# Performance work log

Measured on AMD Instinct MI355X. Metric: run time of the kernel, lower is better.

Reference implementation:

```python
import jax, jax.numpy as jnp
import numpy as np

# LSNNParameters defaults (norse-style)
ALPHA = 100.0            # surrogate sharpness
DT = 1e-3
TAU_SYN_INV = 1.0 / 0.005   # 200
TAU_MEM_INV = 1.0 / 0.01    # 100
TAU_ADAPT_INV = 1.0 / 800.0
V_LEAK = 0.0
V_RESET = 0.0
BETA = 1.8
VTH = 1.0                # sp.vth_init / v_th default


@jax.custom_vjp
def superspike(x):
    # Heaviside forward, SuperSpike surrogate backward ('super' method)
    return (x > 0).astype(x.dtype)

def _ss_fwd(x):
    return superspike(x), x

def _ss_bwd(x, g):
    return (g / (ALPHA * jnp.abs(x) + 1.0) ** 2,)

superspike.defvjp(_ss_fwd, _ss_bwd)


def lsnn_scan(x, w_in, w_rec):
    # x: [T, B, N_in]; w_in: [H, N_in]; w_rec: [H, H]
    T, B, _ = x.shape
    H = w_in.shape[0]
    z0 = jnp.zeros((B, H), x.dtype)
    v0 = jnp.full((B, H), V_LEAK, x.dtype)
    i0 = jnp.zeros((B, H), x.dtype)
    b0 = jnp.full((B, H), VTH, x.dtype)  # mean(v_th)

    def step(carry, xt):
        z, v, i, b = carry
        v_dec = v + DT * TAU_MEM_INV * (V_LEAK - v + i)
        i_dec = i - DT * TAU_SYN_INV * i
        b_dec = b + DT * TAU_ADAPT_INV * (VTH - b)
        z_new = superspike(v_dec - b_dec)
        zd = jax.lax.stop_gradient(z_new)  # reset/adaptation use detached spike
        v_new = (1.0 - zd) * v_dec + zd * V_RESET
        i_new = i_dec + xt @ w_in.T + z @ w_rec.T
        b_new = b_dec + zd * BETA
        return (z_new, v_new, i_new, b_new), z_new

    (zf, vf, i_f, bf), outs = jax.lax.scan(step, (z0, v0, i0, b0), x)
    return outs, (zf, vf, i_f, bf)


def setup_inputs() -> dict:
    key = jax.random.key(0)
    k1, k2, k3 = jax.random.split(key, 3)
    T, B, N_IN, H = 512, 64, 512, 1024
    x = jax.random.normal(k1, (T, B, N_IN), jnp.float32)
    w_in = jax.random.normal(k2, (H, N_IN), jnp.float32) * np.float32(np.sqrt(2.0 / H))
    w_rec = jax.random.normal(k3, (H, H), jnp.float32) * np.float32(np.sqrt(2.0 / H))
    w_rec = w_rec * (1.0 - jnp.eye(H, dtype=jnp.float32))  # autapses=False
    return {"input_tensor": x, "input_weights": w_in, "recurrent_weights": w_rec}


def reference(input_tensor, input_weights, recurrent_weights):
    return lsnn_scan(input_tensor, input_weights, recurrent_weights)
```

## Files before the change

### kernel.cpp

```cpp
#include <hip/hip_runtime.h>

typedef float f32x4 __attribute__((ext_vector_type(4)));

#define T_STEPS 512
#define BATCH   64
#define NIN     512
#define H       1024
#define BH      (BATCH * H)

#define BM 128
#define BN 128
#define BK 16
#define LDSS 132

__global__ void transpose1024(const float* __restrict__ in, float* __restrict__ out) {
    __shared__ float tile[32][33];
    const int tx = threadIdx.x, ty = threadIdx.y;
    const int xg = blockIdx.x * 32 + tx;
    const int ybase = blockIdx.y * 32;
#pragma unroll
    for (int r = 0; r < 32; r += 8)
        tile[ty + r][tx] = in[(size_t)(ybase + ty + r) * H + xg];
    __syncthreads();
    const int x2 = blockIdx.y * 32 + tx;
    const int y2base = blockIdx.x * 32;
#pragma unroll
    for (int r = 0; r < 32; r += 8)
        out[(size_t)(y2base + ty + r) * H + x2] = tile[tx][ty + r];
}

__global__ __launch_bounds__(256) void gemm_xwin(const float* __restrict__ x,
                                                 const float* __restrict__ w,
                                                 float* __restrict__ cur) {
    __shared__ __align__(16) float As[BK][LDSS];
    __shared__ __align__(16) float Bs[BK][LDSS];
    const int tid = threadIdx.x;
    const int tx = tid & 15, ty = tid >> 4;
    const int tx4 = tx * 4, ty4 = ty * 4;
    const int m0 = blockIdx.y * BM;
    const int n0 = blockIdx.x * BN;

    float acc[8][8];
#pragma unroll
    for (int i = 0; i < 8; ++i)
#pragma unroll
        for (int j = 0; j < 8; ++j) acc[i][j] = 0.0f;

    const int ar = tid >> 2;
    const int akc = (tid & 3) * 4;

    for (int k0 = 0; k0 < NIN; k0 += BK) {
        const float4 a0 = *reinterpret_cast<const float4*>(&x[(size_t)(m0 + ar) * NIN + k0 + akc]);
        const float4 a1 = *reinterpret_cast<const float4*>(&x[(size_t)(m0 + ar + 64) * NIN + k0 + akc]);
        const float4 b0 = *reinterpret_cast<const float4*>(&w[(size_t)(n0 + ar) * NIN + k0 + akc]);
        const float4 b1 = *reinterpret_cast<const float4*>(&w[(size_t)(n0 + ar + 64) * NIN + k0 + akc]);
        __syncthreads();
        As[akc + 0][ar] = a0.x; As[akc + 1][ar] = a0.y; As[akc + 2][ar] = a0.z; As[akc + 3][ar] = a0.w;
        As[akc + 0][ar + 64] = a1.x; As[akc + 1][ar + 64] = a1.y; As[akc + 2][ar + 64] = a1.z; As[akc + 3][ar + 64] = a1.w;
        Bs[akc + 0][ar] = b0.x; Bs[akc + 1][ar] = b0.y; Bs[akc + 2][ar] = b0.z; Bs[akc + 3][ar] = b0.w;
        Bs[akc + 0][ar + 64] = b1.x; Bs[akc + 1][ar + 64] = b1.y; Bs[akc + 2][ar + 64] = b1.z; Bs[akc + 3][ar + 64] = b1.w;
        __syncthreads();

#pragma unroll
        for (int kk = 0; kk < BK; ++kk) {
            const float4 av0 = *reinterpret_cast<const float4*>(&As[kk][ty4]);
            const float4 av1 = *reinterpret_cast<const float4*>(&As[kk][ty4 + 64]);
            const float4 bv0 = *reinterpret_cast<const float4*>(&Bs[kk][tx4]);
            const float4 bv1 = *reinterpret_cast<const float4*>(&Bs[kk][tx4 + 64]);
            const float ar_[8] = {av0.x, av0.y, av0.z, av0.w, av1.x, av1.y, av1.z, av1.w};
            const float br_[8] = {bv0.x, bv0.y, bv0.z, bv0.w, bv1.x, bv1.y, bv1.z, bv1.w};
#pragma unroll
            for (int i = 0; i < 8; ++i)
#pragma unroll
                for (int j = 0; j < 8; ++j)
                    acc[i][j] = fmaf(ar_[i], br_[j], acc[i][j]);
        }
    }

#pragma unroll
    for (int gi = 0; gi < 2; ++gi)
#pragma unroll
        for (int ii = 0; ii < 4; ++ii) {
            const int i = gi * 4 + ii;
            const int row = m0 + ty4 + ii + gi * 64;
            float* dst = &cur[(size_t)row * H + n0 + tx4];
            *reinterpret_cast<float4*>(dst)      = make_float4(acc[i][0], acc[i][1], acc[i][2], acc[i][3]);
            *reinterpret_cast<float4*>(dst + 64) = make_float4(acc[i][4], acc[i][5], acc[i][6], acc[i][7]);
        }
}

__global__ __launch_bounds__(256, 1) void lsnn_scan_kernel(float* __restrict__ io,
                                                           const float* __restrict__ wrecT) {
    const int tid = threadIdx.x;
    const int wave = tid >> 6, lane = tid & 63;
    const int j0 = tid * 4;
    const int wq = wave * 256;
    const int b = blockIdx.x;

    __shared__ __align__(16) float ring[3][4][1024];
    __shared__ __align__(16) int list[2][1088];
    __shared__ __align__(16) int cnt[2][4];

    float sv0 = 0.f, sv1 = 0.f, sv2 = 0.f, sv3 = 0.f;
    float si0 = 0.f, si1 = 0.f, si2 = 0.f, si3 = 0.f;
    float sb0 = 1.f, sb1 = 1.f, sb2 = 1.f, sb3 = 1.f;
    float sz0 = 0.f, sz1 = 0.f, sz2 = 0.f, sz3 = 0.f;
    int p = 0;
    int n_carry = 0;

    const float C_MEM = (float)(1e-3 * 100.0);
    const float C_SYN = (float)(1e-3 * 200.0);
    const float C_AD  = (float)(1e-3 * (1.0 / 800.0));
    const float BETA  = 1.8f;

    float* base = io + (size_t)b * H + j0;

    f32x4 P0 = *reinterpret_cast<const f32x4*>(base + (size_t)0 * BH);
    f32x4 P1 = *reinterpret_cast<const f32x4*>(base + (size_t)1 * BH);
    f32x4 P2 = *reinterpret_cast<const f32x4*>(base + (size_t)2 * BH);
    f32x4 P3 = *reinterpret_cast<const f32x4*>(base + (size_t)3 * BH);
    f32x4 P4 = *reinterpret_cast<const f32x4*>(base + (size_t)4 * BH);
    f32x4 P5 = *reinterpret_cast<const f32x4*>(base + (size_t)5 * BH);
    f32x4 P6 = *reinterpret_cast<const f32x4*>(base + (size_t)6 * BH);
    f32x4 P7 = *reinterpret_cast<const f32x4*>(base + (size_t)7 * BH);

#define STAGE(G, SLOT)                                                        \
  { const int A0s_ = (G) << 2;                                                \
    _Pragma("unroll")                                                         \
    for (int rr_ = 0; rr_ < 4; ++rr_) {                                       \
      const int ps_ = A0s_ + rr_;                                             \
      int hs_ = lst[ps_];                                                     \
      hs_ = (ps_ < n) ? hs_ : 0;                                              \
      const float* gp_ = wrecT + (size_t)(unsigned)hs_ * H + wq + lane * 4;   \
      __builtin_amdgcn_global_load_lds(                                       \
          (const __attribute__((address_space(1))) unsigned int*)gp_,         \
          (__attribute__((address_space(3))) unsigned int*)&ring[SLOT][rr_][wq], \
          16, 0, 0);                                                          \
    } }

#define SCAN_STEP(T, CREG, PF)                                                \
  {                                                                           \
    const float cc0 = CREG.x, cc1 = CREG.y, cc2 = CREG.z, cc3 = CREG.w;       \
    const int n = __builtin_amdgcn_readfirstlane(n_carry);                    \
    const int NT = (n + 3) >> 2;                                              \
    const int* lst = &list[p][0];                                             \
     \
    if (NT > 0) STAGE(0, 0);                                                  \
    if (NT > 1) STAGE(1, 1);                                                  \
    if (NT > 2) STAGE(2, 2);                                                  \
                                  \
    const float vd0 = sv0 + C_MEM * (0.0f - sv0 + si0);                       \
    const float vd1 = sv1 + C_MEM * (0.0f - sv1 + si1);                       \
    const float vd2 = sv2 + C_MEM * (0.0f - sv2 + si2);                       \
    const float vd3 = sv3 + C_MEM * (0.0f - sv3 + si3);                       \
    const float id0 = si0 - C_SYN * si0;                                      \
    const float id1 = si1 - C_SYN * si1;                                      \
    const float id2 = si2 - C_SYN * si2;                                      \
    const float id3 = si3 - C_SYN * si3;                                      \
    const float bd0 = sb0 + C_AD * (1.0f - sb0);                              \
    const float bd1 = sb1 + C_AD * (1.0f - sb1);                              \
    const float bd2 = sb2 + C_AD * (1.0f - sb2);                              \
    const float bd3 = sb3 + C_AD * (1.0f - sb3);                              \
    sz0 = ((vd0 - bd0) > 0.0f) ? 1.0f : 0.0f;                                 \
    sz1 = ((vd1 - bd1) > 0.0f) ? 1.0f : 0.0f;                                 \
    sz2 = ((vd2 - bd2) > 0.0f) ? 1.0f : 0.0f;                                 \
    sz3 = ((vd3 - bd3) > 0.0f) ? 1.0f : 0.0f;                                 \
    sv0 = (sz0 > 0.0f) ? 0.0f : vd0;                                          \
    sv1 = (sz1 > 0.0f) ? 0.0f : vd1;                                          \
    sv2 = (sz2 > 0.0f) ? 0.0f : vd2;                                          \
    sv3 = (sz3 > 0.0f) ? 0.0f : vd3;                                          \
    sb0 = (sz0 > 0.0f) ? (bd0 + BETA) : bd0;                                  \
    sb1 = (sz1 > 0.0f) ? (bd1 + BETA) : bd1;                                  \
    sb2 = (sz2 > 0.0f) ? (bd2 + BETA) : bd2;                                  \
    sb3 = (sz3 > 0.0f) ? (bd3 + BETA) : bd3;                                  \
    *reinterpret_cast<f32x4*>(base + (size_t)(T) * BH) =                      \
        (f32x4){sz0, sz1, sz2, sz3};                                          \
    const unsigned long long m0 = __ballot(sz0 > 0.0f);                       \
    const unsigned long long m1 = __ballot(sz1 > 0.0f);                       \
    const unsigned long long m2 = __ballot(sz2 > 0.0f);                       \
    const unsigned long long m3 = __ballot(sz3 > 0.0f);                       \
    unsigned pos = __builtin_amdgcn_mbcnt_hi((unsigned)(m0 >> 32),            \
                   __builtin_amdgcn_mbcnt_lo((unsigned)m0, 0u));              \
    pos = __builtin_amdgcn_mbcnt_hi((unsigned)(m1 >> 32),                     \
          __builtin_amdgcn_mbcnt_lo((unsigned)m1, pos));                      \
    pos = __builtin_amdgcn_mbcnt_hi((unsigned)(m2 >> 32),                     \
          __builtin_amdgcn_mbcnt_lo((unsigned)m2, pos));                      \
    pos = __builtin_amdgcn_mbcnt_hi((unsigned)(m3 >> 32),                     \
          __builtin_amdgcn_mbcnt_lo((unsigned)m3, pos));                      \
    if (lane == 0)                                                            \
      cnt[p ^ 1][wave] = __popcll(m0) + __popcll(m1) + __popcll(m2) + __popcll(m3); \
    asm volatile("s_waitcnt lgkmcnt(0)" ::: "memory");                        \
    __builtin_amdgcn_s_barrier();                                             \
    const int4 nc = *reinterpret_cast<const int4*>(&cnt[p ^ 1][0]);           \
    n_carry = nc.x + nc.y + nc.z + nc.w;                                      \
    const int woff = (wave > 0 ? nc.x : 0) + (wave > 1 ? nc.y : 0) +          \
                     (wave > 2 ? nc.z : 0);                                   \
    int* dst = &list[p ^ 1][woff];                                            \
    if (sz0 > 0.0f) dst[pos++] = j0 + 0;                                      \
    if (sz1 > 0.0f) dst[pos++] = j0 + 1;                                      \
    if (sz2 > 0.0f) dst[pos++] = j0 + 2;                                      \
    if (sz3 > 0.0f) dst[pos++] = j0 + 3;                                      \
    asm volatile("s_waitcnt lgkmcnt(0)" ::: "memory");                        \
    __builtin_amdgcn_s_barrier();                                             \
        \
    float r0 = 0.f, r1 = 0.f, r2 = 0.f, r3 = 0.f;                             \
    {                                                                         \
      int sl = 0;                                                             \
      for (int g = 0; g < NT; ++g) {                                          \
        const int rem = NT - 1 - g;                                           \
        if (rem >= 2)      { asm volatile("s_waitcnt vmcnt(8)" ::: "memory"); } \
        else if (rem == 1) { asm volatile("s_waitcnt vmcnt(4)" ::: "memory"); } \
        else               { asm volatile("s_waitcnt vmcnt(0)" ::: "memory"); } \
        const f32x4 w0 = *reinterpret_cast<const f32x4*>(&ring[sl][0][j0]);   \
        const f32x4 w1 = *reinterpret_cast<const f32x4*>(&ring[sl][1][j0]);   \
        const f32x4 w2 = *reinterpret_cast<const f32x4*>(&ring[sl][2][j0]);   \
        const f32x4 w3 = *reinterpret_cast<const f32x4*>(&ring[sl][3][j0]);   \
        const int gb = g << 2;                                                \
        if (gb + 4 <= n) {                                                    \
          r0 += w0.x; r1 += w0.y; r2 += w0.z; r3 += w0.w;                     \
          r0 += w1.x; r1 += w1.y; r2 += w1.z; r3 += w1.w;                     \
          r0 += w2.x; r1 += w2.y; r2 += w2.z; r3 += w2.w;                     \
          r0 += w3.x; r1 += w3.y; r2 += w3.z; r3 += w3.w;                     \
        } else {                                                              \
          const float ma_ = (gb + 0 < n) ? 1.0f : 0.0f;                       \
          r0 = fmaf(ma_, w0.x, r0); r1 = fmaf(ma_, w0.y, r1);                 \
          r2 = fmaf(ma_, w0.z, r2); r3 = fmaf(ma_, w0.w, r3);                 \
          const float mb_ = (gb + 1 < n) ? 1.0f : 0.0f;                       \
          r0 = fmaf(mb_, w1.x, r0); r1 = fmaf(mb_, w1.y, r1);                 \
          r2 = fmaf(mb_, w1.z, r2); r3 = fmaf(mb_, w1.w, r3);                 \
          const float mc_ = (gb + 2 < n) ? 1.0f : 0.0f;                       \
          r0 = fmaf(mc_, w2.x, r0); r1 = fmaf(mc_, w2.y, r1);                 \
          r2 = fmaf(mc_, w2.z, r2); r3 = fmaf(mc_, w2.w, r3);                 \
          const float md_ = (gb + 3 < n) ? 1.0f : 0.0f;                       \
          r0 = fmaf(md_, w3.x, r0); r1 = fmaf(md_, w3.y, r1);                 \
          r2 = fmaf(md_, w3.z, r2); r3 = fmaf(md_, w3.w, r3);                 \
        }                                                                     \
        if (g + 3 < NT) {                                                     \
             \
          asm volatile("s_waitcnt lgkmcnt(0)" ::: "memory");                  \
          STAGE(g + 3, sl);                                                   \
        }                                                                     \
        sl = (sl == 2) ? 0 : sl + 1;                                          \
      }                                                                       \
    }                                                                         \
    if (PF) {                                                                 \
      if ((T) + 1 < T_STEPS) {                                                \
        const float* pb = base + (size_t)((T) + 1) * BH;                      \
        P0 = *(const f32x4*)(pb + (size_t)0 * BH);                            \
        P1 = *(const f32x4*)(pb + (size_t)1 * BH);                            \
        P2 = *(const f32x4*)(pb + (size_t)2 * BH);                            \
        P3 = *(const f32x4*)(pb + (size_t)3 * BH);                            \
        P4 = *(const f32x4*)(pb + (size_t)4 * BH);                            \
        P5 = *(const f32x4*)(pb + (size_t)5 * BH);                            \
        P6 = *(const f32x4*)(pb + (size_t)6 * BH);                            \
        P7 = *(const f32x4*)(pb + (size_t)7 * BH);                            \
      }                                                                       \
    }                                                                         \
    si0 = (id0 + cc0) + r0;                                                   \
    si1 = (id1 + cc1) + r1;                                                   \
    si2 = (id2 + cc2) + r2;                                                   \
    si3 = (id3 + cc3) + r3;                                                   \
    p ^= 1;                                                                   \
  }

    for (int t = 0; t < T_STEPS; t += 8) {
        SCAN_STEP(t,     P0, 0);
        SCAN_STEP(t + 1, P1, 0);
        SCAN_STEP(t + 2, P2, 0);
        SCAN_STEP(t + 3, P3, 0);
        SCAN_STEP(t + 4, P4, 0);
        SCAN_STEP(t + 5, P5, 0);
        SCAN_STEP(t + 6, P6, 0);
        SCAN_STEP(t + 7, P7, 1);
    }
#undef SCAN_STEP
#undef STAGE

    float* fo = io + (size_t)T_STEPS * BH + (size_t)b * H + j0;
    *reinterpret_cast<float4*>(fo)          = make_float4(sz0, sz1, sz2, sz3);
    *reinterpret_cast<float4*>(fo + BH)     = make_float4(sv0, sv1, sv2, sv3);
    *reinterpret_cast<float4*>(fo + 2 * BH) = make_float4(si0, si1, si2, si3);
    *reinterpret_cast<float4*>(fo + 3 * BH) = make_float4(sb0, sb1, sb2, sb3);
}

extern "C" void kernel_launch(void* const* d_in, const int* in_sizes, int n_in,
                              void* d_out, int out_size, void* d_ws, size_t ws_size,
                              hipStream_t stream) {
    const float* x     = (const float*)d_in[0];
    const float* w_in  = (const float*)d_in[1];
    const float* w_rec = (const float*)d_in[2];
    float* out   = (float*)d_out;
    float* wrecT = (float*)d_ws;

    transpose1024<<<dim3(H / 32, H / 32), dim3(32, 8), 0, stream>>>(w_rec, wrecT);
    gemm_xwin<<<dim3(H / BN, (T_STEPS * BATCH) / BM), 256, 0, stream>>>(x, w_in, out);
    lsnn_scan_kernel<<<BATCH, 256, 0, stream>>>(out, wrecT);
}
```

Measured before the change: 755.4 us.

## Widen spike-row gather groups to eight rows and prefetch GEMM tiles

The recurrent scan now gathers eight active w_rec rows per ring slot instead of four. This doubles the bytes in flight per stage and halves the number of wait/accumulate iterations, with the vmcnt thresholds adjusted to match. The input-projection GEMM also gets register prefetch: it loads the next K tile's global values before the compute loop, so global latency overlaps with the FMAs. The larger ring uses more LDS, and the tail groups waste more masked work when the spike count is not a multiple of eight.

```diff
diff --git a/kernel.cpp b/kernel.cpp
--- a/kernel.cpp
+++ b/kernel.cpp
@@ -49,17 +49,24 @@
     const int ar = tid >> 2;
     const int akc = (tid & 3) * 4;
 
+    float4 a0 = *reinterpret_cast<const float4*>(&x[(size_t)(m0 + ar) * NIN + akc]);
+    float4 a1 = *reinterpret_cast<const float4*>(&x[(size_t)(m0 + ar + 64) * NIN + akc]);
+    float4 b0 = *reinterpret_cast<const float4*>(&w[(size_t)(n0 + ar) * NIN + akc]);
+    float4 b1 = *reinterpret_cast<const float4*>(&w[(size_t)(n0 + ar + 64) * NIN + akc]);
+
     for (int k0 = 0; k0 < NIN; k0 += BK) {
-        const float4 a0 = *reinterpret_cast<const float4*>(&x[(size_t)(m0 + ar) * NIN + k0 + akc]);
-        const float4 a1 = *reinterpret_cast<const float4*>(&x[(size_t)(m0 + ar + 64) * NIN + k0 + akc]);
-        const float4 b0 = *reinterpret_cast<const float4*>(&w[(size_t)(n0 + ar) * NIN + k0 + akc]);
-        const float4 b1 = *reinterpret_cast<const float4*>(&w[(size_t)(n0 + ar + 64) * NIN + k0 + akc]);
         __syncthreads();
         As[akc + 0][ar] = a0.x; As[akc + 1][ar] = a0.y; As[akc + 2][ar] = a0.z; As[akc + 3][ar] = a0.w;
         As[akc + 0][ar + 64] = a1.x; As[akc + 1][ar + 64] = a1.y; As[akc + 2][ar + 64] = a1.z; As[akc + 3][ar + 64] = a1.w;
         Bs[akc + 0][ar] = b0.x; Bs[akc + 1][ar] = b0.y; Bs[akc + 2][ar] = b0.z; Bs[akc + 3][ar] = b0.w;
         Bs[akc + 0][ar + 64] = b1.x; Bs[akc + 1][ar + 64] = b1.y; Bs[akc + 2][ar + 64] = b1.z; Bs[akc + 3][ar + 64] = b1.w;
         __syncthreads();
+
+        const int kn = (k0 + BK < NIN) ? (k0 + BK) : 0;
+        a0 = *reinterpret_cast<const float4*>(&x[(size_t)(m0 + ar) * NIN + kn + akc]);
+        a1 = *reinterpret_cast<const float4*>(&x[(size_t)(m0 + ar + 64) * NIN + kn + akc]);
+        b0 = *reinterpret_cast<const float4*>(&w[(size_t)(n0 + ar) * NIN + kn + akc]);
+        b1 = *reinterpret_cast<const float4*>(&w[(size_t)(n0 + ar + 64) * NIN + kn + akc]);
 
 #pragma unroll
         for (int kk = 0; kk < BK; ++kk) {
@@ -97,7 +104,7 @@
     const int wq = wave * 256;
     const int b = blockIdx.x;
 
-    __shared__ __align__(16) float ring[3][4][1024];
+    __shared__ __align__(16) float ring[3][8][1024];
     __shared__ __align__(16) int list[2][1088];
     __shared__ __align__(16) int cnt[2][4];
 
@@ -125,9 +132,9 @@
     f32x4 P7 = *reinterpret_cast<const f32x4*>(base + (size_t)7 * BH);
 
 #define STAGE(G, SLOT)                                                        \
-  { const int A0s_ = (G) << 2;                                                \
+  { const int A0s_ = (G) << 3;                                                \
     _Pragma("unroll")                                                         \
-    for (int rr_ = 0; rr_ < 4; ++rr_) {                                       \
+    for (int rr_ = 0; rr_ < 8; ++rr_) {                                       \
       const int ps_ = A0s_ + rr_;                                             \
       int hs_ = lst[ps_];                                                     \
       hs_ = (ps_ < n) ? hs_ : 0;                                              \
@@ -138,11 +145,17 @@
           16, 0, 0);                                                          \
     } }
 
+#define ACCROW(WREG) { r0 += WREG.x; r1 += WREG.y; r2 += WREG.z; r3 += WREG.w; }
+#define ACCROWM(WREG, POS)                                                    \
+  { const float mm_ = ((POS) < n) ? 1.0f : 0.0f;                              \
+    r0 = fmaf(mm_, WREG.x, r0); r1 = fmaf(mm_, WREG.y, r1);                   \
+    r2 = fmaf(mm_, WREG.z, r2); r3 = fmaf(mm_, WREG.w, r3); }
+
 #define SCAN_STEP(T, CREG, PF)                                                \
   {                                                                           \
     const float cc0 = CREG.x, cc1 = CREG.y, cc2 = CREG.z, cc3 = CREG.w;       \
     const int n = __builtin_amdgcn_readfirstlane(n_carry);                    \
-    const int NT = (n + 3) >> 2;                                              \
+    const int NT = (n + 7) >> 3;                                              \
     const int* lst = &list[p][0];                                             \
      \
     if (NT > 0) STAGE(0, 0);                                                  \
@@ -208,35 +221,29 @@
       int sl = 0;                                                             \
       for (int g = 0; g < NT; ++g) {                                          \
         const int rem = NT - 1 - g;                                           \
-        if (rem >= 2)      { asm volatile("s_waitcnt vmcnt(8)" ::: "memory"); } \
-        else if (rem == 1) { asm volatile("s_waitcnt vmcnt(4)" ::: "memory"); } \
+        if (rem >= 2)      { asm volatile("s_waitcnt vmcnt(16)" ::: "memory"); } \
+        else if (rem == 1) { asm volatile("s_waitcnt vmcnt(8)" ::: "memory"); } \
         else               { asm volatile("s_waitcnt vmcnt(0)" ::: "memory"); } \
         const f32x4 w0 = *reinterpret_cast<const f32x4*>(&ring[sl][0][j0]);   \
         const f32x4 w1 = *reinterpret_cast<const f32x4*>(&ring[sl][1][j0]);   \
         const f32x4 w2 = *reinterpret_cast<const f32x4*>(&ring[sl][2][j0]);   \
         const f32x4 w3 = *reinterpret_cast<const f32x4*>(&ring[sl][3][j0]);   \
-        const int gb = g << 2;                                                \
-        if (gb + 4 <= n) {                                                    \
-          r0 += w0.x; r1 += w0.y; r2 += w0.z; r3 += w0.w;                     \
-          r0 += w1.x; r1 += w1.y; r2 += w1.z; r3 += w1.w;                     \
-          r0 += w2.x; r1 += w2.y; r2 += w2.z; r3 += w2.w;                     \
-          r0 += w3.x; r1 += w3.y; r2 += w3.z; r3 += w3.w;                     \
+        const f32x4 w4 = *reinterpret_cast<const f32x4*>(&ring[sl][4][j0]);   \
+        const f32x4 w5 = *reinterpret_cast<const f32x4*>(&ring[sl][5][j0]);   \
+        const f32x4 w6 = *reinterpret_cast<const f32x4*>(&ring[sl][6][j0]);   \
+        const f32x4 w7 = *reinterpret_cast<const f32x4*>(&ring[sl][7][j0]);   \
+        const int gb = g << 3;                                                \
+        if (gb + 8 <= n) {                                                    \
+          ACCROW(w0) ACCROW(w1) ACCROW(w2) ACCROW(w3)                         \
+          ACCROW(w4) ACCROW(w5) ACCROW(w6) ACCROW(w7)                         \
         } else {                                                              \
-          const float ma_ = (gb + 0 < n) ? 1.0f : 0.0f;                       \
-          r0 = fmaf(ma_, w0.x, r0); r1 = fmaf(ma_, w0.y, r1);                 \
-          r2 = fmaf(ma_, w0.z, r2); r3 = fmaf(ma_, w0.w, r3);                 \
-          const float mb_ = (gb + 1 < n) ? 1.0f : 0.0f;                       \
-          r0 = fmaf(mb_, w1.x, r0); r1 = fmaf(mb_, w1.y, r1);                 \
-          r2 = fmaf(mb_, w1.z, r2); r3 = fmaf(mb_, w1.w, r3);                 \
-          const float mc_ = (gb + 2 < n) ? 1.0f : 0.0f;                       \
-          r0 = fmaf(mc_, w2.x, r0); r1 = fmaf(mc_, w2.y, r1);                 \
-          r2 = fmaf(mc_, w2.z, r2); r3 = fmaf(mc_, w2.w, r3);                 \
-          const float md_ = (gb + 3 < n) ? 1.0f : 0.0f;                       \
-          r0 = fmaf(md_, w3.x, r0); r1 = fmaf(md_, w3.y, r1);                 \
-          r2 = fmaf(md_, w3.z, r2); r3 = fmaf(md_, w3.w, r3);                 \
+          ACCROWM(w0, gb + 0) ACCROWM(w1, gb + 1)                             \
+          ACCROWM(w2, gb + 2) ACCROWM(w3, gb + 3)                             \
+          ACCROWM(w4, gb + 4) ACCROWM(w5, gb + 5)                             \
+          ACCROWM(w6, gb + 6) ACCROWM(w7, gb + 7)                             \
         }                                                                     \
         if (g + 3 < NT) {                                                     \
-             \
+               \
           asm volatile("s_waitcnt lgkmcnt(0)" ::: "memory");                  \
           STAGE(g + 3, sl);                                                   \
         }                                                                     \
@@ -274,6 +281,8 @@
         SCAN_STEP(t + 7, P7, 1);
     }
 #undef SCAN_STEP
+#undef ACCROWM
+#undef ACCROW
 #undef STAGE
 
     float* fo = io + (size_t)T_STEPS * BH + (size_t)b * H + j0;
```

Measured after the change: 780.6 us. 1.03x slower.
